# Kernel tuning notes

Hardware: AMD Instinct MI355X
Metric: run time of the kernel (lower is better)

## Reference

```python
import jax, jax.numpy as jnp
import numpy as np

B = 2048
NUM_FIELDS = 32
EMBED = 64
P = NUM_FIELDS * (NUM_FIELDS - 1) // 2  # 496 field pairs

# Pair indices (i < j), identical to the row_idx/col_idx loops in __init__
_ROW, _COL = np.triu_indices(NUM_FIELDS, k=1)
ROW_IDX = jnp.asarray(_ROW, dtype=jnp.int32)
COL_IDX = jnp.asarray(_COL, dtype=jnp.int32)


def setup_inputs() -> dict:
    key = jax.random.key(0)
    k1, k2 = jax.random.split(key)
    emb_inputs = jax.random.normal(k1, (B, NUM_FIELDS, EMBED), dtype=jnp.float32)
    # kernel_type='mat' -> kernel shape (E, P, E), xavier_normal-like init
    fan_in = P * EMBED
    fan_out = EMBED
    std = float(np.sqrt(2.0 / (fan_in + fan_out)))
    kernel = jax.random.normal(k2, (EMBED, P, EMBED), dtype=jnp.float32) * std
    return {"emb_inputs": emb_inputs, "kernel": kernel}


def reference(emb_inputs, kernel):
    # Gather field pairs: p, q shape (B, P, E)
    p = emb_inputs[:, ROW_IDX]
    q = emb_inputs[:, COL_IDX]
    # torch named-tensor chain for kernel_type='mat':
    #   kp[b, h, n] = sum_e p[b, n, e] * kernel[h, n, e]
    #   out[b, n]   = sum_h kp[b, h, n] * q[b, n, h]
    # Fused: out[b, n] = sum_{e, h} p[b, n, e] * kernel[h, n, e] * q[b, n, h]
    return jnp.einsum('bne,hne,bnh->bn', p, kernel, q)
```

## Files before the change

kernel.cpp:

```cpp
#include <hip/hip_runtime.h>


#define B_TOT 2048
#define NF    32
#define EMB   64
#define NP    496
#define BT    32
#define ESTR  72

typedef short bf16x8 __attribute__((ext_vector_type(8)));
typedef short bf16x4 __attribute__((ext_vector_type(4)));
typedef float f32x4  __attribute__((ext_vector_type(4)));

static __device__ inline unsigned f2bf(float f) {
    unsigned u = __builtin_bit_cast(unsigned, f);
    u += 0x7fffu + ((u >> 16) & 1u);
    return u >> 16;
}
static __device__ inline unsigned pack2(float lo, float hi) {
    return f2bf(lo) | (f2bf(hi) << 16);
}
static __device__ inline float bf2f(short s) {
    return __builtin_bit_cast(float, (unsigned)((unsigned short)s) << 16);
}

__global__ __launch_bounds__(256) void cvt2(const float* __restrict__ kern,
                                            short* __restrict__ kb) {
    const int n = blockIdx.x;
    __shared__ short w[EMB * ESTR];
#pragma unroll
    for (int j = 0; j < 4; ++j) {
        const int idx = threadIdx.x + 256 * j;
        const int h = idx >> 4, e4 = idx & 15;
        const f32x4 v = *(const f32x4*)(kern + ((size_t)h * NP + n) * EMB + e4 * 4);
        uint2 u;
        u.x = pack2(v[0], v[1]);
        u.y = pack2(v[2], v[3]);
        *(uint2*)&w[h * ESTR + e4 * 4] = u;
    }
    __syncthreads();
#pragma unroll
    for (int j = 0; j < 2; ++j) {
        const int u    = threadIdx.x + 256 * j;
        const int frag = u >> 6, l = u & 63;
        const int h  = (frag >> 1) * 16 + (l & 15);
        const int e0 = (frag & 1) * 32 + (l >> 4) * 8;
        const bf16x8 t = *(const bf16x8*)&w[h * ESTR + e0];
        *(bf16x8*)(kb + (size_t)n * 4096 + u * 8) = t;
    }
}

__global__ __launch_bounds__(512, 4) void opnl_main(
    const float* __restrict__ emb,
    const short* __restrict__ kb,
    float* __restrict__ out)
{
    __shared__ short elds[16 * BT * ESTR];

    const int type = blockIdx.x >> 6;
    const int bt   = blockIdx.x & 63;
    const int b0   = bt * BT;

    int bLo, bHi, npr;
    switch (type) {
        case 0: case 1: bLo = 0;  bHi = 0;  npr = 60; break;
        case 2: case 3: bLo = 16; bHi = 16; npr = 60; break;
        case 4:         bLo = 0;  bHi = 8;  npr = 64; break;
        case 5:         bLo = 8;  bHi = 16; npr = 64; break;
        case 6:         bLo = 0;  bHi = 16; npr = 64; break;
        default:        bLo = 8;  bHi = 8;  npr = 64; break;
    }

    {
        const int sb = threadIdx.x >> 4;
        const int e4 = threadIdx.x & 15;
#pragma unroll
        for (int f = 0; f < 16; ++f) {
            const int gf = f + (f < 8 ? bLo : bHi);
            const f32x4 v = *(const f32x4*)(emb + ((size_t)(b0 + sb) * NF + gf) * EMB + e4 * 4);
            uint2 u;
            u.x = pack2(v[0], v[1]);
            u.y = pack2(v[2], v[3]);
            *(uint2*)&elds[(f * BT + sb) * ESTR + e4 * 4] = u;
        }
    }
    __syncthreads();

    const int lane = threadIdx.x & 63;
    const int wid  = threadIdx.x >> 6;
    const int lo4  = lane & 15;
    const int hi4  = lane >> 4;

    auto pairK = [&](int k, int& lr, int& lc, int& nn) {
        int pr = wid + 8 * k;
        if (pr >= npr) pr -= npr;
        if (type < 4) {
            int pig = (type & 1) * 60 + pr;
            int r = 0;
            while (pig >= 15 - r) { pig -= 15 - r; ++r; }
            lr = r; lc = r + 1 + pig;
        } else {
            lr = pr >> 3; lc = 8 + (pr & 7);
        }
        const int R = lr + (lr < 8 ? bLo : bHi);
        const int C = lc + (lc < 8 ? bLo : bHi);
        nn = R * (63 - R) / 2 + (C - R - 1);
    };

    auto loadW = [&](bf16x8 (&wf)[4][2], int nn) {
        const bf16x8* wp = (const bf16x8*)(kb + (size_t)nn * 4096);
#pragma unroll
        for (int mh = 0; mh < 4; ++mh)
#pragma unroll
            for (int kc = 0; kc < 2; ++kc)
                wf[mh][kc] = wp[(mh * 2 + kc) * 64 + lane];
    };

    auto compute = [&](bf16x8 (&wf)[4][2], int lr, int lc, int nn) {
#pragma unroll
        for (int sub = 0; sub < 2; ++sub) {
            const int bb = sub * 16 + lo4;

            bf16x8 pf[2];
#pragma unroll
            for (int kc = 0; kc < 2; ++kc)
                pf[kc] = *(const bf16x8*)&elds[(lr * BT + bb) * ESTR + kc * 32 + hi4 * 8];

            f32x4 acc[4] = {f32x4{0,0,0,0}, f32x4{0,0,0,0},
                            f32x4{0,0,0,0}, f32x4{0,0,0,0}};
#pragma unroll
            for (int mh = 0; mh < 4; ++mh)
#pragma unroll
                for (int kc = 0; kc < 2; ++kc)
                    acc[mh] = __builtin_amdgcn_mfma_f32_16x16x32_bf16(
                        wf[mh][kc], pf[kc], acc[mh], 0, 0, 0);

            float val = 0.f;
#pragma unroll
            for (int mh = 0; mh < 4; ++mh) {
                const bf16x4 q = *(const bf16x4*)&elds[(lc * BT + bb) * ESTR + mh * 16 + hi4 * 4];
                val += acc[mh][0] * bf2f(q[0]) + acc[mh][1] * bf2f(q[1])
                     + acc[mh][2] * bf2f(q[2]) + acc[mh][3] * bf2f(q[3]);
            }
            val += __shfl_xor(val, 16, 64);
            val += __shfl_xor(val, 32, 64);
            if (lane < 16) out[(size_t)(b0 + bb) * NP + nn] = val;
        }
    };

    bf16x8 wA[4][2], wB[4][2];
    int lrA, lcA, nA, lrB, lcB, nB;
    pairK(0, lrA, lcA, nA);
    loadW(wA, nA);
#pragma unroll
    for (int k = 0; k < 8; ++k) {
        if ((k & 1) == 0) {
            if (k < 7) { pairK(k + 1, lrB, lcB, nB); loadW(wB, nB); }
            compute(wA, lrA, lcA, nA);
        } else {
            if (k < 7) { pairK(k + 1, lrA, lcA, nA); loadW(wA, nA); }
            compute(wB, lrB, lcB, nB);
        }
    }
}

extern "C" void kernel_launch(void* const* d_in, const int* in_sizes, int n_in,
                              void* d_out, int out_size, void* d_ws, size_t ws_size,
                              hipStream_t stream) {
    const float* emb  = (const float*)d_in[0];
    const float* kern = (const float*)d_in[1];
    float*       out  = (float*)d_out;
    short*       kb   = (short*)d_ws;

    cvt2<<<NP, 256, 0, stream>>>(kern, kb);
    opnl_main<<<8 * 64, 512, 0, stream>>>(emb, kb, out);
}
```

Before: 30.41 us.

## Pre-convert embeddings to swizzled bf16 and stream them into LDS with direct loads

Result: faster. 29.17 us (-4.1%).

```diff
diff --git a/kernel.cpp b/kernel.cpp
--- a/kernel.cpp
+++ b/kernel.cpp
@@ -6,7 +6,6 @@
 #define EMB   64
 #define NP    496
 #define BT    32
-#define ESTR  72
 
 typedef short bf16x8 __attribute__((ext_vector_type(8)));
 typedef short bf16x4 __attribute__((ext_vector_type(4)));
@@ -24,38 +23,59 @@
     return __builtin_bit_cast(float, (unsigned)((unsigned short)s) << 16);
 }
 
-__global__ __launch_bounds__(256) void cvt2(const float* __restrict__ kern,
-                                            short* __restrict__ kb) {
-    const int n = blockIdx.x;
-    __shared__ short w[EMB * ESTR];
-#pragma unroll
-    for (int j = 0; j < 4; ++j) {
-        const int idx = threadIdx.x + 256 * j;
-        const int h = idx >> 4, e4 = idx & 15;
-        const f32x4 v = *(const f32x4*)(kern + ((size_t)h * NP + n) * EMB + e4 * 4);
-        uint2 u;
-        u.x = pack2(v[0], v[1]);
-        u.y = pack2(v[2], v[3]);
-        *(uint2*)&w[h * ESTR + e4 * 4] = u;
-    }
-    __syncthreads();
-#pragma unroll
-    for (int j = 0; j < 2; ++j) {
-        const int u    = threadIdx.x + 256 * j;
-        const int frag = u >> 6, l = u & 63;
-        const int h  = (frag >> 1) * 16 + (l & 15);
-        const int e0 = (frag & 1) * 32 + (l >> 4) * 8;
-        const bf16x8 t = *(const bf16x8*)&w[h * ESTR + e0];
-        *(bf16x8*)(kb + (size_t)n * 4096 + u * 8) = t;
+#define AS1 __attribute__((address_space(1)))
+#define AS3 __attribute__((address_space(3)))
+
+__global__ __launch_bounds__(256) void prep(const float* __restrict__ kern,
+                                            const float* __restrict__ emb,
+                                            short* __restrict__ kb,
+                                            short* __restrict__ ebf) {
+    __shared__ short w[EMB * 72];
+    if (blockIdx.x < NP) {
+        const int n = blockIdx.x;
+#pragma unroll
+        for (int j = 0; j < 4; ++j) {
+            const int idx = threadIdx.x + 256 * j;
+            const int h = idx >> 4, e4 = idx & 15;
+            const f32x4 v = *(const f32x4*)(kern + ((size_t)h * NP + n) * EMB + e4 * 4);
+            uint2 u;
+            u.x = pack2(v[0], v[1]);
+            u.y = pack2(v[2], v[3]);
+            *(uint2*)&w[h * 72 + e4 * 4] = u;
+        }
+        __syncthreads();
+#pragma unroll
+        for (int j = 0; j < 2; ++j) {
+            const int u    = threadIdx.x + 256 * j;
+            const int frag = u >> 6, l = u & 63;
+            const int h  = (frag >> 1) * 16 + (l & 15);
+            const int e0 = (frag & 1) * 32 + (l >> 4) * 8;
+            const bf16x8 t = *(const bf16x8*)&w[h * 72 + e0];
+            *(bf16x8*)(kb + (size_t)n * 4096 + u * 8) = t;
+        }
+    } else {
+        const int t    = (blockIdx.x - NP) * 256 + threadIdx.x;
+        const int cidx = t & 127;
+        const int f    = (t >> 7) & 31;
+        const int bt16 = t >> 12;
+        const int bp = cidx >> 3, x = cidx & 7;
+        const int ec = x ^ (bp & 7);
+        const float* src = emb + (((size_t)(bt16 * 16 + bp) * NF + f) * EMB + ec * 8);
+        const f32x4 a = *(const f32x4*)src;
+        const f32x4 b = *(const f32x4*)(src + 4);
+        uint4 u;
+        u.x = pack2(a[0], a[1]); u.y = pack2(a[2], a[3]);
+        u.z = pack2(b[0], b[1]); u.w = pack2(b[2], b[3]);
+        *(uint4*)(ebf + (size_t)t * 8) = u;
     }
 }
 
 __global__ __launch_bounds__(512, 4) void opnl_main(
-    const float* __restrict__ emb,
+    const short* __restrict__ ebf,
     const short* __restrict__ kb,
     float* __restrict__ out)
 {
-    __shared__ short elds[16 * BT * ESTR];
+    __shared__ short elds[16 * 2 * 1024];
 
     const int type = blockIdx.x >> 6;
     const int bt   = blockIdx.x & 63;
@@ -71,25 +91,23 @@
         default:        bLo = 8;  bHi = 8;  npr = 64; break;
     }
 
-    {
-        const int sb = threadIdx.x >> 4;
-        const int e4 = threadIdx.x & 15;
-#pragma unroll
-        for (int f = 0; f < 16; ++f) {
-            const int gf = f + (f < 8 ? bLo : bHi);
-            const f32x4 v = *(const f32x4*)(emb + ((size_t)(b0 + sb) * NF + gf) * EMB + e4 * 4);
-            uint2 u;
-            u.x = pack2(v[0], v[1]);
-            u.y = pack2(v[2], v[3]);
-            *(uint2*)&elds[(f * BT + sb) * ESTR + e4 * 4] = u;
-        }
-    }
-    __syncthreads();
-
     const int lane = threadIdx.x & 63;
     const int wid  = threadIdx.x >> 6;
     const int lo4  = lane & 15;
     const int hi4  = lane >> 4;
+
+#pragma unroll
+    for (int i = 0; i < 4; ++i) {
+        const int s   = wid * 4 + i;
+        const int lf  = s >> 1, sub = s & 1;
+        const int gf  = lf + (lf < 8 ? bLo : bHi);
+        const short* src = ebf + ((size_t)((bt * 2 + sub) * 32 + gf)) * 1024;
+        __builtin_amdgcn_global_load_lds((const AS1 void*)(src + lane * 8),
+                                         (AS3 void*)&elds[s * 1024], 16, 0, 0);
+        __builtin_amdgcn_global_load_lds((const AS1 void*)(src + 512 + lane * 8),
+                                         (AS3 void*)&elds[s * 1024 + 512], 16, 0, 0);
+    }
+    __syncthreads();
 
     auto pairK = [&](int k, int& lr, int& lc, int& nn) {
         int pr = wid + 8 * k;
@@ -124,7 +142,9 @@
             bf16x8 pf[2];
 #pragma unroll
             for (int kc = 0; kc < 2; ++kc)
-                pf[kc] = *(const bf16x8*)&elds[(lr * BT + bb) * ESTR + kc * 32 + hi4 * 8];
+                pf[kc] = *(const bf16x8*)
+                    &elds[(lr * 2 + sub) * 1024 +
+                          (lo4 * 8 + (((kc * 4 + hi4) ^ (lo4 & 7)))) * 8];
 
             f32x4 acc[4] = {f32x4{0,0,0,0}, f32x4{0,0,0,0},
                             f32x4{0,0,0,0}, f32x4{0,0,0,0}};
@@ -138,7 +158,10 @@
             float val = 0.f;
 #pragma unroll
             for (int mh = 0; mh < 4; ++mh) {
-                const bf16x4 q = *(const bf16x4*)&elds[(lc * BT + bb) * ESTR + mh * 16 + hi4 * 4];
+                const bf16x4 q = *(const bf16x4*)
+                    &elds[(lc * 2 + sub) * 1024 +
+                          (lo4 * 8 + (((mh * 2 + (hi4 >> 1)) ^ (lo4 & 7)))) * 8 +
+                          (hi4 & 1) * 4];
                 val += acc[mh][0] * bf2f(q[0]) + acc[mh][1] * bf2f(q[1])
                      + acc[mh][2] * bf2f(q[2]) + acc[mh][3] * bf2f(q[3]);
             }
@@ -170,8 +193,10 @@
     const float* emb  = (const float*)d_in[0];
     const float* kern = (const float*)d_in[1];
     float*       out  = (float*)d_out;
-    short*       kb   = (short*)d_ws;
-
-    cvt2<<<NP, 256, 0, stream>>>(kern, kb);
-    opnl_main<<<8 * 64, 512, 0, stream>>>(emb, kb, out);
-}
+
+    short* kb  = (short*)d_ws;
+    short* ebf = (short*)((char*)d_ws + (4 << 20));
+
+    prep<<<NP + (B_TOT * NF * EMB / 8) / 256, 256, 0, stream>>>(kern, emb, kb, ebf);
+    opnl_main<<<8 * 64, 512, 0, stream>>>(ebf, kb, out);
+}
```
